# Kernel optimization log

Hardware: AMD Instinct MI355X
Metric: run time of the kernel (lower is better)

Reference implementation:

```python
import jax, jax.numpy as jnp
import numpy as np

P = 16; D = 256; NH = 8; L = 4; E = 8; K = 2; B = 32; IMG = 224; NC = 1000; FF = 4 * D
N = (IMG // P) ** 2  # 196 patches
HD = D // NH  # head dim
EPS = 1e-5


def setup_inputs():
    key = jax.random.key(0)
    ks = iter(jax.random.split(key, 16))
    s = 0.02  # init scale keeps softmax/logits well-conditioned
    rn = lambda shape: jax.random.normal(next(ks), shape, jnp.float32) * s
    return dict(
        x=jax.random.normal(next(ks), (B, 3, IMG, IMG), jnp.float32),
        patch_w=rn((3 * P * P, D)), patch_b=jnp.zeros((D,), jnp.float32),
        cls_token=rn((1, 1, D)), pos_embed=rn((1, N + 1, D)),
        router_w=rn((L, D, E)), router_b=jnp.zeros((L, E), jnp.float32),
        ln1_g=jnp.ones((L, E, D), jnp.float32), ln1_b=jnp.zeros((L, E, D), jnp.float32),
        qkv_w=rn((L, E, D, 3 * D)), qkv_b=jnp.zeros((L, E, 3 * D), jnp.float32),
        proj_w=rn((L, E, D, D)), proj_b=jnp.zeros((L, E, D), jnp.float32),
        ln2_g=jnp.ones((L, E, D), jnp.float32), ln2_b=jnp.zeros((L, E, D), jnp.float32),
        fc1_w=rn((L, E, D, FF)), fc1_b=jnp.zeros((L, E, FF), jnp.float32),
        fc2_w=rn((L, E, FF, D)), fc2_b=jnp.zeros((L, E, D), jnp.float32),
        norm_g=jnp.ones((D,), jnp.float32), norm_b=jnp.zeros((D,), jnp.float32),
        head_w=rn((D, NC)), head_b=jnp.zeros((NC,), jnp.float32),
    )


def _ln(x, g, b):
    m = x.mean(-1, keepdims=True)
    v = ((x - m) ** 2).mean(-1, keepdims=True)
    return (x - m) * jax.lax.rsqrt(v + EPS) * g + b


def _block(x, g1, b1, wqkv, bqkv, wp, bp, g2, b2, w1, bias1, w2, bias2):
    # standard ViT block: LN -> MHA -> residual, LN -> MLP(GELU) -> residual
    bsz, S, _ = x.shape
    h = _ln(x, g1, b1)
    qkv = (h @ wqkv + bqkv).reshape(bsz, S, 3, NH, HD)
    q, k, v = qkv[:, :, 0], qkv[:, :, 1], qkv[:, :, 2]  # [B,S,NH,HD]
    scores = jnp.einsum('bqhd,bkhd->bhqk', q, k) / np.float32(np.sqrt(HD))
    attn = jax.nn.softmax(scores, axis=-1)
    o = jnp.einsum('bhqk,bkhd->bqhd', attn, v).reshape(bsz, S, D)
    x = x + o @ wp + bp
    h2 = _ln(x, g2, b2)
    x = x + jax.nn.gelu(h2 @ w1 + bias1, approximate=False) @ w2 + bias2
    return x


def _moe_layer(x, rw, rb, g1, b1, wqkv, bqkv, wp, bp, g2, b2, w1, bias1, w2, bias2):
    probs = jax.nn.softmax(x @ rw + rb, axis=-1)            # [B,S,E]
    topv, topi = jax.lax.top_k(probs, K)                    # [B,S,K]
    topv = topv / topv.sum(-1, keepdims=True)
    # dense all-expert compute (faithful to source), vmapped over experts
    eo = jax.vmap(_block, in_axes=(None,) + (0,) * 12)(
        x, g1, b1, wqkv, bqkv, wp, bp, g2, b2, w1, bias1, w2, bias2)  # [E,B,S,D]
    eo = jnp.moveaxis(eo, 0, 2)                             # [B,S,E,D]
    sel = jnp.take_along_axis(eo, topi[..., None], axis=2)  # [B,S,K,D]
    return (sel * topv[..., None]).sum(axis=2)


def reference(x, patch_w, patch_b, cls_token, pos_embed, router_w, router_b,
              ln1_g, ln1_b, qkv_w, qkv_b, proj_w, proj_b, ln2_g, ln2_b,
              fc1_w, fc1_b, fc2_w, fc2_b, norm_g, norm_b, head_w, head_b):
    bsz = x.shape[0]
    g = IMG // P
    # patch embed: stride==kernel conv == patch extraction + matmul
    patches = x.reshape(bsz, 3, g, P, g, P).transpose(0, 2, 4, 1, 3, 5).reshape(bsz, N, 3 * P * P)
    h = patches @ patch_w + patch_b                          # [B,N,D]
    cls = jnp.broadcast_to(cls_token, (bsz, 1, D))
    h = jnp.concatenate([cls, h], axis=1) + pos_embed        # [B,N+1,D]
    for l in range(L):
        h = _moe_layer(h, router_w[l], router_b[l], ln1_g[l], ln1_b[l],
                       qkv_w[l], qkv_b[l], proj_w[l], proj_b[l], ln2_g[l], ln2_b[l],
                       fc1_w[l], fc1_b[l], fc2_w[l], fc2_b[l])
    h = _ln(h, norm_g, norm_b)
    return h[:, 0] @ head_w + head_b                         # [B,NC]
```

## Files before the change

### kernel.cpp

```cpp
#include <hip/hip_runtime.h>
#include <math.h>

#define SEQ 197
#define BATCH 32
#define DIM 256
#define NHEAD 8
#define HDIM 32
#define NEXP 8
#define NLAYER 4
#define FFDIM 1024
#define NCLS 1000
#define NPATCH 196
#define TOK (BATCH * SEQ)
#define CAP 13120
#define YB 99

__device__ __forceinline__ void gload16(const float* g, float* l) {
  __builtin_amdgcn_global_load_lds(
      (const __attribute__((address_space(1))) void*)g,
      (__attribute__((address_space(3))) void*)l, 16, 0, 0);
}

__global__ __launch_bounds__(256) void k_im2col(const float* __restrict__ x,
                                                float* __restrict__ Apat) {
  int idx = blockIdx.x * 256 + threadIdx.x;
  if (idx >= BATCH * NPATCH * 768) return;
  int cpp = idx % 768;
  int m = idx / 768;
  int n = m % NPATCH;
  int b = m / NPATCH;
  int c = cpp >> 8;
  int py = (cpp >> 4) & 15;
  int px = cpp & 15;
  int gy = n / 14, gx = n % 14;
  Apat[idx] = x[(((size_t)b * 3 + c) * 224 + gy * 16 + py) * 224 + gx * 16 + px];
}

__global__ __launch_bounds__(256) void k_foldw(const float* __restrict__ qw,
                                               const float* __restrict__ g1,
                                               float* __restrict__ w4) {
  size_t idx = (size_t)blockIdx.x * 256 + threadIdx.x;
  if (idx >= (size_t)32 * 256 * 768) return;
  size_t kn = idx % (256 * 768);
  int le = (int)(idx / (256 * 768));
  int k = (int)(kn / 768);
  w4[idx] = qw[idx] * g1[le * 256 + k];
}

__global__ __launch_bounds__(256) void k_foldb(const float* __restrict__ qw,
                                               const float* __restrict__ qb,
                                               const float* __restrict__ b1,
                                               float* __restrict__ b4) {
  int le = blockIdx.y;
  int col = blockIdx.x * 256 + threadIdx.x;
  const float* w = qw + (size_t)le * 256 * 768 + col;
  const float* lb = b1 + (size_t)le * 256;
  float acc = 0.f;
  for (int k = 0; k < 256; ++k) acc = fmaf(lb[k], w[(size_t)k * 768], acc);
  b4[(size_t)le * 768 + col] = acc + qb[(size_t)le * 768 + col];
}

__global__ __launch_bounds__(256) void k_gemm_t(
    const float* __restrict__ A, const float* __restrict__ W,
    const float* __restrict__ bias, const float* __restrict__ R,
    const float* __restrict__ X2, const float* __restrict__ PW,
    const int* __restrict__ ptok, const int* __restrict__ off_e,
    const int* __restrict__ cnt_e, float* __restrict__ out, int M, int N,
    int K, int Wld, int wcol, int bstride, int ebase, int mode, int flags) {
  __shared__ float As[2][16][68];
  __shared__ float Bs[2][16][128];
  int gx = gridDim.x, gy = gridDim.y;
  int nwg = gx * gy * gridDim.z;
  int lin = blockIdx.x + gx * (blockIdx.y + gy * blockIdx.z);
  int q8 = nwg >> 3, r8 = nwg & 7;
  int xcd = lin & 7, jj0 = lin >> 3;
  int nlin = (xcd < r8 ? xcd * (q8 + 1) : r8 * (q8 + 1) + (xcd - r8) * q8) + jj0;
  int bx = nlin % gx;
  int t1 = nlin / gx;
  int by = t1 % gy;
  int bz = t1 / gy;

  int e = ebase + bz;
  bool seg = (flags & 1) != 0;
  int rows = seg ? cnt_e[e] : M;
  int row0 = by * 64;
  if (row0 >= rows) return;
  int col0 = bx * 128;
  int tid = threadIdx.x;
  int base = seg ? off_e[e] : 0;
  const float* Wp = W + (size_t)e * K * Wld + wcol;
  const float* bp = bias + (size_t)e * bstride + wcol;

  int rr = tid >> 2, kq = (tid & 3) * 4;
  int r = row0 + rr;
  bool val = r < rows;
  int rc = val ? r : rows - 1;
  int gr0 = base + rc;
  int arow = seg ? ((flags & 2) ? ptok[gr0] : gr0) : rc;
  const float* aptr = A + (size_t)arow * K + kq;
  float msk = val ? 1.f : 0.f;
  int wv = tid >> 6, lane = tid & 63;
  const float* bsrc0 =
      Wp + (size_t)(2 * wv + (lane >> 5)) * Wld + col0 + (lane & 31) * 4;
  const float* bsrc1 = bsrc0 + (size_t)8 * Wld;

  gload16(bsrc0, &Bs[0][2 * wv][0]);
  gload16(bsrc1, &Bs[0][8 + 2 * wv][0]);
  {
    float4 av = *(const float4*)aptr;
    As[0][kq + 0][rr] = av.x * msk;
    As[0][kq + 1][rr] = av.y * msk;
    As[0][kq + 2][rr] = av.z * msk;
    As[0][kq + 3][rr] = av.w * msk;
  }
  __syncthreads();

  int tx = tid & 15, ty = tid >> 4;
  float acc0[4][4] = {};
  float acc1[4][4] = {};
  int cur = 0;
  for (int k0 = 0; k0 < K; k0 += 16) {
    int nb = cur ^ 1;
    bool more = (k0 + 16) < K;
    float4 av;
    if (more) {
      av = *(const float4*)(aptr + k0 + 16);
      gload16(bsrc0 + (size_t)(k0 + 16) * Wld, &Bs[nb][2 * wv][0]);
      gload16(bsrc1 + (size_t)(k0 + 16) * Wld, &Bs[nb][8 + 2 * wv][0]);
    }
#pragma unroll
    for (int k = 0; k < 16; ++k) {
      float4 a = *(const float4*)&As[cur][k][ty * 4];
      float4 b0 = *(const float4*)&Bs[cur][k][tx * 4];
      float4 b1 = *(const float4*)&Bs[cur][k][64 + tx * 4];
      float aa[4] = {a.x, a.y, a.z, a.w};
      float b0a[4] = {b0.x, b0.y, b0.z, b0.w};
      float b1a[4] = {b1.x, b1.y, b1.z, b1.w};
#pragma unroll
      for (int i = 0; i < 4; ++i)
#pragma unroll
        for (int j = 0; j < 4; ++j) {
          acc0[i][j] = fmaf(aa[i], b0a[j], acc0[i][j]);
          acc1[i][j] = fmaf(aa[i], b1a[j], acc1[i][j]);
        }
    }
    if (more) {
      As[nb][kq + 0][rr] = av.x * msk;
      As[nb][kq + 1][rr] = av.y * msk;
      As[nb][kq + 2][rr] = av.z * msk;
      As[nb][kq + 3][rr] = av.w * msk;
    }
    __syncthreads();
    cur = nb;
  }
#pragma unroll
  for (int i = 0; i < 4; ++i) {
    int rrow = row0 + ty * 4 + i;
    if (rrow >= rows) continue;
    int gr = base + rrow;
#pragma unroll
    for (int c = 0; c < 2; ++c) {
#pragma unroll
      for (int j = 0; j < 4; ++j) {
        int col = col0 + c * 64 + tx * 4 + j;
        float v = (c ? acc1[i][j] : acc0[i][j]) + bp[col];
        if (mode == 0) {
          size_t orow = seg ? (size_t)gr : (size_t)bz * M + rrow;
          out[orow * N + col] = v;
        } else if (mode == 1) {
          int t = ptok[gr];
          out[(size_t)gr * N + col] = v + R[(size_t)t * N + col];
        } else if (mode == 2) {
          out[(size_t)gr * N + col] =
              0.5f * v * (1.f + erff(v * 0.70710678118654752f));
        } else {
          int t = ptok[gr];
          atomicAdd(&out[(size_t)t * N + col],
                    PW[gr] * (X2[(size_t)gr * N + col] + v));
        }
      }
    }
  }
}

__global__ __launch_bounds__(256) void k_assemble(const float* __restrict__ tmp,
                                                  const float* __restrict__ cls,
                                                  const float* __restrict__ pos,
                                                  float* __restrict__ h) {
  int idx = blockIdx.x * 256 + threadIdx.x;
  if (idx >= TOK * DIM) return;
  int d = idx & 255;
  int t = idx >> 8;
  int s = t % SEQ;
  int b = t / SEQ;
  float v = (s == 0) ? cls[d] : tmp[((size_t)b * NPATCH + s - 1) * DIM + d];
  h[idx] = v + pos[s * DIM + d];
}

__global__ __launch_bounds__(64) void k_router(
    const float* __restrict__ h, const float* __restrict__ rw,
    const float* __restrict__ rb, int* __restrict__ cnt_eb,
    int* __restrict__ tmp_s, float* __restrict__ tmp_w) {
  int t = blockIdx.x;
  int lane = threadIdx.x;
  float hv[4];
  const float* hp = h + (size_t)t * DIM + lane * 4;
#pragma unroll
  for (int i = 0; i < 4; i++) hv[i] = hp[i];
  float lg[8];
#pragma unroll
  for (int e = 0; e < 8; e++) {
    float p = 0.f;
#pragma unroll
    for (int i = 0; i < 4; i++) p = fmaf(hv[i], rw[(lane * 4 + i) * 8 + e], p);
#pragma unroll
    for (int off = 32; off; off >>= 1) p += __shfl_down(p, off);
    lg[e] = p;
  }
  if (lane == 0) {
#pragma unroll
    for (int e = 0; e < 8; e++) lg[e] += rb[e];
    float mx = lg[0];
#pragma unroll
    for (int e = 1; e < 8; e++) mx = fmaxf(mx, lg[e]);
    float pr[8];
#pragma unroll
    for (int e = 0; e < 8; e++) pr[e] = expf(lg[e] - mx);
    int i0 = 0;
#pragma unroll
    for (int e = 1; e < 8; e++)
      if (pr[e] > pr[i0]) i0 = e;
    int i1 = -1;
#pragma unroll
    for (int e = 0; e < 8; e++)
      if (e != i0 && (i1 < 0 || pr[e] > pr[i1])) i1 = e;
    float wsum = pr[i0] + pr[i1];
    int b = t / SEQ, s = t - b * SEQ;
    int eb0 = i0 * 32 + b;
    int p0 = atomicAdd(&cnt_eb[eb0], 1);
    tmp_s[eb0 * SEQ + p0] = s;
    tmp_w[eb0 * SEQ + p0] = pr[i0] / wsum;
    int eb1 = i1 * 32 + b;
    int p1 = atomicAdd(&cnt_eb[eb1], 1);
    tmp_s[eb1 * SEQ + p1] = s;
    tmp_w[eb1 * SEQ + p1] = pr[i1] / wsum;
  }
}

__global__ __launch_bounds__(64) void k_scan(const int* __restrict__ cnt_eb,
                                             int* __restrict__ off_eb,
                                             int* __restrict__ off_e,
                                             int* __restrict__ cnt_e) {
  if (threadIdx.x == 0 && blockIdx.x == 0) {
    int g = 0;
    for (int e = 0; e < 8; e++) {
      off_e[e] = g;
      int ce = 0;
      for (int b = 0; b < 32; b++) {
        off_eb[e * 32 + b] = g + ce;
        ce += cnt_eb[e * 32 + b];
      }
      cnt_e[e] = ce;
      g += (ce + 63) & ~63;
    }
  }
}

__global__ __launch_bounds__(256) void k_scatter(
    const int* __restrict__ cnt_eb, const int* __restrict__ off_eb,
    const int* __restrict__ tmp_s, const float* __restrict__ tmp_w,
    int* __restrict__ ptok, float* __restrict__ pw) {
  int eb = blockIdx.x;
  int b = eb & 31;
  int c = cnt_eb[eb];
  int o = off_eb[eb];
  for (int i = threadIdx.x; i < c; i += 256) {
    ptok[o + i] = b * SEQ + tmp_s[eb * SEQ + i];
    pw[o + i] = tmp_w[eb * SEQ + i];
  }
}

__global__ __launch_bounds__(256) void k_ln_noaff(const float* __restrict__ X,
                                                  float* __restrict__ Y) {
  int t = blockIdx.x;
  int d = threadIdx.x;
  float v = X[(size_t)t * DIM + d];
  __shared__ float red[4];
  float s = v;
#pragma unroll
  for (int o = 32; o; o >>= 1) s += __shfl_down(s, o);
  if ((d & 63) == 0) red[d >> 6] = s;
  __syncthreads();
  float mean = (red[0] + red[1] + red[2] + red[3]) * (1.f / 256.f);
  __syncthreads();
  float c = v - mean;
  float s2 = c * c;
#pragma unroll
  for (int o = 32; o; o >>= 1) s2 += __shfl_down(s2, o);
  if ((d & 63) == 0) red[d >> 6] = s2;
  __syncthreads();
  float var = (red[0] + red[1] + red[2] + red[3]) * (1.f / 256.f);
  Y[(size_t)t * DIM + d] = c * rsqrtf(var + 1e-5f);
}

__global__ __launch_bounds__(256) void k_ln_seg(
    const float* __restrict__ X, const float* __restrict__ g,
    const float* __restrict__ bta, float* __restrict__ Y,
    const int* __restrict__ off_e, const int* __restrict__ cnt_e) {
  int e = blockIdx.y;
  int cnt = cnt_e[e];
  int base = off_e[e];
  int d = threadIdx.x;
  float gv = g[e * DIM + d];
  float bv = bta[e * DIM + d];
  __shared__ float red[4];
  for (int r = blockIdx.x; r < cnt; r += gridDim.x) {
    size_t gr = (size_t)(base + r);
    float v = X[gr * DIM + d];
    float s = v;
#pragma unroll
    for (int o = 32; o; o >>= 1) s += __shfl_down(s, o);
    if ((d & 63) == 0) red[d >> 6] = s;
    __syncthreads();
    float mean = (red[0] + red[1] + red[2] + red[3]) * (1.f / 256.f);
    __syncthreads();
    float c = v - mean;
    float s2 = c * c;
#pragma unroll
    for (int o = 32; o; o >>= 1) s2 += __shfl_down(s2, o);
    if ((d & 63) == 0) red[d >> 6] = s2;
    __syncthreads();
    float var = (red[0] + red[1] + red[2] + red[3]) * (1.f / 256.f);
    Y[gr * DIM + d] = c * rsqrtf(var + 1e-5f) * gv + bv;
    __syncthreads();
  }
}

__global__ __launch_bounds__(256) void k_attn(
    const float* __restrict__ qc, const float* __restrict__ kv,
    float* __restrict__ oc, const int* __restrict__ cnt_eb,
    const int* __restrict__ off_eb, int ebase) {
  int bx = blockIdx.x;
  int hh = bx & 7;
  int b = (bx >> 3) & 31;
  int ez = bx >> 8;
  int eb = (ebase + ez) * 32 + b;
  int cnt = cnt_eb[eb];
  if (cnt == 0) return;
  int off = off_eb[eb];
  __shared__ float Ks[SEQ][HDIM];
  __shared__ float Vs[SEQ][HDIM];
  const float* base = kv + ((size_t)ez * TOK + (size_t)b * SEQ) * 512;
  int tid = threadIdx.x;
  for (int i = tid; i < SEQ * 8; i += 256) {
    int row = i >> 3, c4 = (i & 7) * 4;
    const float* kp = base + (size_t)row * 512 + hh * HDIM + c4;
    *(float4*)&Ks[row][c4] = *(const float4*)kp;
    *(float4*)&Vs[row][c4] = *(const float4*)(kp + 256);
  }
  __syncthreads();
  int grp = tid >> 2;
  int ln = tid & 3;
  for (int qi = grp; qi < cnt; qi += 64) {
    const float* qp = qc + (size_t)(off + qi) * DIM + hh * HDIM + ln * 8;
    float4 q0 = *(const float4*)qp;
    float4 q1 = *(const float4*)(qp + 4);
    float qv[8] = {q0.x, q0.y, q0.z, q0.w, q1.x, q1.y, q1.z, q1.w};
    float m = -1e30f, l = 0.f;
    float acc[8] = {};
    for (int j = 0; j < SEQ; ++j) {
      const float4* kr = (const float4*)&Ks[j][ln * 8];
      float4 k0 = kr[0], k1 = kr[1];
      float s = qv[0] * k0.x;
      s = fmaf(qv[1], k0.y, s);
      s = fmaf(qv[2], k0.z, s);
      s = fmaf(qv[3], k0.w, s);
      s = fmaf(qv[4], k1.x, s);
      s = fmaf(qv[5], k1.y, s);
      s = fmaf(qv[6], k1.z, s);
      s = fmaf(qv[7], k1.w, s);
      s += __shfl_xor(s, 1);
      s += __shfl_xor(s, 2);
      s *= 0.17677669529663687f;
      float e2;
      if (s > m) {
        float f = expf(m - s);
        l *= f;
#pragma unroll
        for (int d = 0; d < 8; ++d) acc[d] *= f;
        m = s;
        e2 = 1.f;
      } else {
        e2 = expf(s - m);
      }
      l += e2;
      const float4* vr = (const float4*)&Vs[j][ln * 8];
      float4 v0 = vr[0], v1 = vr[1];
      acc[0] = fmaf(e2, v0.x, acc[0]);
      acc[1] = fmaf(e2, v0.y, acc[1]);
      acc[2] = fmaf(e2, v0.z, acc[2]);
      acc[3] = fmaf(e2, v0.w, acc[3]);
      acc[4] = fmaf(e2, v1.x, acc[4]);
      acc[5] = fmaf(e2, v1.y, acc[5]);
      acc[6] = fmaf(e2, v1.z, acc[6]);
      acc[7] = fmaf(e2, v1.w, acc[7]);
    }
    float inv = 1.f / l;
    float* op = oc + (size_t)(off + qi) * DIM + hh * HDIM + ln * 8;
    float4 o0 = {acc[0] * inv, acc[1] * inv, acc[2] * inv, acc[3] * inv};
    float4 o1 = {acc[4] * inv, acc[5] * inv, acc[6] * inv, acc[7] * inv};
    *(float4*)op = o0;
    *(float4*)(op + 4) = o1;
  }
}

__global__ __launch_bounds__(256) void k_head(const float* __restrict__ h,
                                              const float* __restrict__ ng,
                                              const float* __restrict__ nb,
                                              const float* __restrict__ hw,
                                              const float* __restrict__ hb,
                                              float* __restrict__ out) {
  int b = blockIdx.x;
  int d = threadIdx.x;
  float v = h[(size_t)b * SEQ * DIM + d];
  __shared__ float red[4];
  __shared__ float hls[DIM];
  float s = v;
#pragma unroll
  for (int off = 32; off; off >>= 1) s += __shfl_down(s, off);
  if ((d & 63) == 0) red[d >> 6] = s;
  __syncthreads();
  float mean = (red[0] + red[1] + red[2] + red[3]) * (1.f / 256.f);
  __syncthreads();
  float c = v - mean;
  float s2 = c * c;
#pragma unroll
  for (int off = 32; off; off >>= 1) s2 += __shfl_down(s2, off);
  if ((d & 63) == 0) red[d >> 6] = s2;
  __syncthreads();
  float var = (red[0] + red[1] + red[2] + red[3]) * (1.f / 256.f);
  hls[d] = c * rsqrtf(var + 1e-5f) * ng[d] + nb[d];
  __syncthreads();
  for (int j = d; j < NCLS; j += 256) {
    float sdot = hb[j];
    for (int k2 = 0; k2 < DIM; k2++)
      sdot = fmaf(hls[k2], hw[(size_t)k2 * NCLS + j], sdot);
    out[(size_t)b * NCLS + j] = sdot;
  }
}

extern "C" void kernel_launch(void* const* d_in, const int* in_sizes, int n_in,
                              void* d_out, int out_size, void* d_ws,
                              size_t ws_size, hipStream_t stream) {
  const float* x = (const float*)d_in[0];
  const float* patch_w = (const float*)d_in[1];
  const float* patch_b = (const float*)d_in[2];
  const float* cls_token = (const float*)d_in[3];
  const float* pos_embed = (const float*)d_in[4];
  const float* router_w = (const float*)d_in[5];
  const float* router_b = (const float*)d_in[6];
  const float* ln1_g = (const float*)d_in[7];
  const float* ln1_b = (const float*)d_in[8];
  const float* qkv_w = (const float*)d_in[9];
  const float* qkv_b = (const float*)d_in[10];
  const float* proj_w = (const float*)d_in[11];
  const float* proj_b = (const float*)d_in[12];
  const float* ln2_g = (const float*)d_in[13];
  const float* ln2_b = (const float*)d_in[14];
  const float* fc1_w = (const float*)d_in[15];
  const float* fc1_b = (const float*)d_in[16];
  const float* fc2_w = (const float*)d_in[17];
  const float* fc2_b = (const float*)d_in[18];
  const float* norm_g = (const float*)d_in[19];
  const float* norm_b = (const float*)d_in[20];
  const float* head_w = (const float*)d_in[21];
  const float* head_b = (const float*)d_in[22];

  float* ws = (float*)d_ws;
  size_t off = 0;
  float* xhat = ws + off; off += (size_t)TOK * DIM;
  float* hbuf = ws + off; off += (size_t)TOK * DIM;
  float* accb = ws + off; off += (size_t)TOK * DIM;
  float* qc   = ws + off; off += (size_t)CAP * DIM;
  float* oc   = ws + off; off += (size_t)CAP * DIM;
  float* x2c  = ws + off; off += (size_t)CAP * DIM;
  float* ffc  = ws + off; off += (size_t)CAP * FFDIM;
  float* w4   = ws + off; off += (size_t)32 * DIM * 768;
  float* b4   = ws + off; off += (size_t)32 * 768;
  float* pwb  = ws + off; off += CAP;
  float* tmpw = ws + off; off += 256 * SEQ;
  int* ptok   = (int*)(ws + off); off += CAP;
  int* tmps   = (int*)(ws + off); off += 256 * SEQ;
  int* cnt_eb = (int*)(ws + off); off += 256;
  int* off_eb = (int*)(ws + off); off += 256;
  int* off_e  = (int*)(ws + off); off += 8;
  int* cnt_e  = (int*)(ws + off); off += 8;
  float* kv4 = ffc;
  float* hlnc = qc;

  k_foldw<<<(32 * 256 * 768 + 255) / 256, 256, 0, stream>>>(qkv_w, ln1_g, w4);
  k_foldb<<<dim3(3, 32), 256, 0, stream>>>(qkv_w, qkv_b, ln1_b, b4);

  int tot = BATCH * NPATCH * 768;
  k_im2col<<<(tot + 255) / 256, 256, 0, stream>>>(x, ffc);
  k_gemm_t<<<dim3(2, 98, 1), 256, 0, stream>>>(
      ffc, patch_w, patch_b, nullptr, nullptr, nullptr, nullptr, nullptr,
      nullptr, qc, BATCH * NPATCH, DIM, 768, DIM, 0, 0, 0, 0, 0);
  k_assemble<<<(TOK * DIM + 255) / 256, 256, 0, stream>>>(qc, cls_token,
                                                          pos_embed, hbuf);

  float* h = hbuf;
  float* acc = accb;
  for (int l = 0; l < NLAYER; ++l) {
    hipMemsetAsync(acc, 0, (size_t)TOK * DIM * sizeof(float), stream);
    hipMemsetAsync(cnt_eb, 0, 256 * sizeof(int), stream);
    k_router<<<TOK, 64, 0, stream>>>(h, router_w + (size_t)l * DIM * NEXP,
                                     router_b + (size_t)l * NEXP, cnt_eb, tmps,
                                     tmpw);
    k_scan<<<1, 64, 0, stream>>>(cnt_eb, off_eb, off_e, cnt_e);
    k_scatter<<<256, 256, 0, stream>>>(cnt_eb, off_eb, tmps, tmpw, ptok, pwb);
    k_ln_noaff<<<TOK, 256, 0, stream>>>(h, xhat);

    const float* Wl = w4 + (size_t)l * NEXP * DIM * 768;
    const float* Bl = b4 + (size_t)l * NEXP * 768;

    k_gemm_t<<<dim3(2, YB, 8), 256, 0, stream>>>(
        xhat, Wl, Bl, nullptr, nullptr, nullptr, ptok, off_e, cnt_e, qc, 0,
        DIM, DIM, 768, 0, 768, 0, 0, 3);

    for (int grp = 0; grp < 2; ++grp) {
      int eb0 = grp * 4;
      k_gemm_t<<<dim3(4, YB, 4), 256, 0, stream>>>(
          xhat, Wl, Bl, nullptr, nullptr, nullptr, nullptr, nullptr, nullptr,
          kv4, TOK, 512, DIM, 768, 256, 768, eb0, 0, 0);
      k_attn<<<1024, 256, 0, stream>>>(qc, kv4, oc, cnt_eb, off_eb, eb0);
    }

    k_gemm_t<<<dim3(2, YB, 8), 256, 0, stream>>>(
        oc, proj_w + (size_t)l * NEXP * DIM * DIM,
        proj_b + (size_t)l * NEXP * DIM, h, nullptr, nullptr, ptok, off_e,
        cnt_e, x2c, 0, DIM, DIM, DIM, 0, DIM, 0, 1, 1);
    k_ln_seg<<<dim3(YB, 8), 256, 0, stream>>>(
        x2c, ln2_g + (size_t)l * NEXP * DIM, ln2_b + (size_t)l * NEXP * DIM,
        hlnc, off_e, cnt_e);
    k_gemm_t<<<dim3(8, YB, 8), 256, 0, stream>>>(
        hlnc, fc1_w + (size_t)l * NEXP * DIM * FFDIM,
        fc1_b + (size_t)l * NEXP * FFDIM, nullptr, nullptr, nullptr, ptok,
        off_e, cnt_e, ffc, 0, FFDIM, DIM, FFDIM, 0, FFDIM, 0, 2, 1);
    k_gemm_t<<<dim3(2, YB, 8), 256, 0, stream>>>(
        ffc, fc2_w + (size_t)l * NEXP * FFDIM * DIM,
        fc2_b + (size_t)l * NEXP * DIM, nullptr, x2c, pwb, ptok, off_e, cnt_e,
        acc, 0, DIM, FFDIM, DIM, 0, DIM, 0, 3, 1);
    float* t = h;
    h = acc;
    acc = t;
  }
  k_head<<<BATCH, 256, 0, stream>>>(h, norm_g, norm_b, head_w, head_b,
                                    (float*)d_out);
}
```

Baseline: 3.587 ms.

## Tile K/V over 64-key chunks in attention and make online softmax branchless

```diff
diff --git a/kernel.cpp b/kernel.cpp
--- a/kernel.cpp
+++ b/kernel.cpp
@@ -14,6 +14,7 @@
 #define TOK (BATCH * SEQ)
 #define CAP 13120
 #define YB 99
+#define KT 64
 
 __device__ __forceinline__ void gload16(const float* g, float* l) {
   __builtin_amdgcn_global_load_lds(
@@ -348,69 +349,78 @@
   int cnt = cnt_eb[eb];
   if (cnt == 0) return;
   int off = off_eb[eb];
-  __shared__ float Ks[SEQ][HDIM];
-  __shared__ float Vs[SEQ][HDIM];
+  __shared__ float Ks[KT][HDIM];
+  __shared__ float Vs[KT][HDIM];
   const float* base = kv + ((size_t)ez * TOK + (size_t)b * SEQ) * 512;
   int tid = threadIdx.x;
-  for (int i = tid; i < SEQ * 8; i += 256) {
-    int row = i >> 3, c4 = (i & 7) * 4;
-    const float* kp = base + (size_t)row * 512 + hh * HDIM + c4;
-    *(float4*)&Ks[row][c4] = *(const float4*)kp;
-    *(float4*)&Vs[row][c4] = *(const float4*)(kp + 256);
-  }
-  __syncthreads();
   int grp = tid >> 2;
   int ln = tid & 3;
-  for (int qi = grp; qi < cnt; qi += 64) {
-    const float* qp = qc + (size_t)(off + qi) * DIM + hh * HDIM + ln * 8;
+  int nrounds = (cnt + 63) >> 6;
+  for (int qr = 0; qr < nrounds; ++qr) {
+    int qi = qr * 64 + grp;
+    bool act = qi < cnt;
+    int qc_i = act ? qi : cnt - 1;
+    const float* qp = qc + (size_t)(off + qc_i) * DIM + hh * HDIM + ln * 8;
     float4 q0 = *(const float4*)qp;
     float4 q1 = *(const float4*)(qp + 4);
     float qv[8] = {q0.x, q0.y, q0.z, q0.w, q1.x, q1.y, q1.z, q1.w};
     float m = -1e30f, l = 0.f;
     float acc[8] = {};
-    for (int j = 0; j < SEQ; ++j) {
-      const float4* kr = (const float4*)&Ks[j][ln * 8];
-      float4 k0 = kr[0], k1 = kr[1];
-      float s = qv[0] * k0.x;
-      s = fmaf(qv[1], k0.y, s);
-      s = fmaf(qv[2], k0.z, s);
-      s = fmaf(qv[3], k0.w, s);
-      s = fmaf(qv[4], k1.x, s);
-      s = fmaf(qv[5], k1.y, s);
-      s = fmaf(qv[6], k1.z, s);
-      s = fmaf(qv[7], k1.w, s);
-      s += __shfl_xor(s, 1);
-      s += __shfl_xor(s, 2);
-      s *= 0.17677669529663687f;
-      float e2;
-      if (s > m) {
-        float f = expf(m - s);
-        l *= f;
-#pragma unroll
-        for (int d = 0; d < 8; ++d) acc[d] *= f;
-        m = s;
-        e2 = 1.f;
-      } else {
-        e2 = expf(s - m);
+    for (int t0 = 0; t0 < SEQ; t0 += KT) {
+      int nk = (SEQ - t0) < KT ? (SEQ - t0) : KT;
+      __syncthreads();
+      for (int i = tid; i < nk * 16; i += 256) {
+        int row = i >> 4, half = (i >> 3) & 1, c4 = (i & 7) * 4;
+        const float* p =
+            base + (size_t)(t0 + row) * 512 + half * 256 + hh * HDIM + c4;
+        if (half == 0)
+          *(float4*)&Ks[row][c4] = *(const float4*)p;
+        else
+          *(float4*)&Vs[row][c4] = *(const float4*)p;
       }
-      l += e2;
-      const float4* vr = (const float4*)&Vs[j][ln * 8];
-      float4 v0 = vr[0], v1 = vr[1];
-      acc[0] = fmaf(e2, v0.x, acc[0]);
-      acc[1] = fmaf(e2, v0.y, acc[1]);
-      acc[2] = fmaf(e2, v0.z, acc[2]);
-      acc[3] = fmaf(e2, v0.w, acc[3]);
-      acc[4] = fmaf(e2, v1.x, acc[4]);
-      acc[5] = fmaf(e2, v1.y, acc[5]);
-      acc[6] = fmaf(e2, v1.z, acc[6]);
-      acc[7] = fmaf(e2, v1.w, acc[7]);
-    }
-    float inv = 1.f / l;
-    float* op = oc + (size_t)(off + qi) * DIM + hh * HDIM + ln * 8;
-    float4 o0 = {acc[0] * inv, acc[1] * inv, acc[2] * inv, acc[3] * inv};
-    float4 o1 = {acc[4] * inv, acc[5] * inv, acc[6] * inv, acc[7] * inv};
-    *(float4*)op = o0;
-    *(float4*)(op + 4) = o1;
+      __syncthreads();
+      const float* KsL = &Ks[0][ln * 8];
+      const float* VsL = &Vs[0][ln * 8];
+#pragma unroll 2
+      for (int j = 0; j < nk; ++j) {
+        const float4* kr = (const float4*)(KsL + j * HDIM);
+        float4 k0 = kr[0], k1 = kr[1];
+        float s = qv[0] * k0.x;
+        s = fmaf(qv[1], k0.y, s);
+        s = fmaf(qv[2], k0.z, s);
+        s = fmaf(qv[3], k0.w, s);
+        s = fmaf(qv[4], k1.x, s);
+        s = fmaf(qv[5], k1.y, s);
+        s = fmaf(qv[6], k1.z, s);
+        s = fmaf(qv[7], k1.w, s);
+        s += __shfl_xor(s, 1);
+        s += __shfl_xor(s, 2);
+        s *= 0.17677669529663687f;
+        float nm = fmaxf(m, s);
+        float f = expf(m - nm);
+        float e2 = expf(s - nm);
+        m = nm;
+        l = fmaf(l, f, e2);
+        const float4* vr = (const float4*)(VsL + j * HDIM);
+        float4 v0 = vr[0], v1 = vr[1];
+        acc[0] = fmaf(acc[0], f, e2 * v0.x);
+        acc[1] = fmaf(acc[1], f, e2 * v0.y);
+        acc[2] = fmaf(acc[2], f, e2 * v0.z);
+        acc[3] = fmaf(acc[3], f, e2 * v0.w);
+        acc[4] = fmaf(acc[4], f, e2 * v1.x);
+        acc[5] = fmaf(acc[5], f, e2 * v1.y);
+        acc[6] = fmaf(acc[6], f, e2 * v1.z);
+        acc[7] = fmaf(acc[7], f, e2 * v1.w);
+      }
+    }
+    if (act) {
+      float inv = 1.f / l;
+      float* op = oc + (size_t)(off + qi) * DIM + hh * HDIM + ln * 8;
+      float4 o0 = {acc[0] * inv, acc[1] * inv, acc[2] * inv, acc[3] * inv};
+      float4 o1 = {acc[4] * inv, acc[5] * inv, acc[6] * inv, acc[7] * inv};
+      *(float4*)op = o0;
+      *(float4*)(op + 4) = o1;
+    }
   }
 }
 
```

After: 3.362 ms. 6.3% less time.
